# Kernel tuning notes

Hardware: AMD Instinct MI355X
Metric: run time of the kernel (lower is better)

Reference implementation:

```python
import jax, jax.numpy as jnp
import numpy as np
import math

S, D = 8192, 128

def setup_inputs() -> dict:
    key = jax.random.key(0)
    kq, kk, kv = jax.random.split(key, 3)
    return {
        "q": jax.random.normal(kq, (S, D), dtype=jnp.float32),
        "k": jax.random.normal(kk, (S, D), dtype=jnp.float32),
        "v": jax.random.normal(kv, (S, D), dtype=jnp.float32),
    }

def reference(q, k, v):
    # scores: [S, S]; scale by sqrt(d) as in the torch module
    scale = 1.0 / math.sqrt(q.shape[1])
    scores = (q @ k.T) * scale
    attn = jax.nn.softmax(scores, axis=-1)
    return attn @ v
```

## Files before the change

### kernel.cpp

```cpp
#include <hip/hip_runtime.h>
#include <hip/hip_bf16.h>

#define SEQ 8192
#define HD 128
#define BM 128
#define BN 64
#define NQT (SEQ / BM)
#define THREADS 512

typedef __bf16 bf16_t;
typedef __bf16 bf16x2 __attribute__((ext_vector_type(2)));
typedef __bf16 bf16x8 __attribute__((ext_vector_type(8)));
typedef float f32x4 __attribute__((ext_vector_type(4)));
typedef float f32x16 __attribute__((ext_vector_type(16)));
typedef unsigned int u32x4 __attribute__((ext_vector_type(4)));

#if __has_builtin(__builtin_amdgcn_exp2f)
__device__ inline float exp2_fast(float x) { return __builtin_amdgcn_exp2f(x); }
#else
__device__ inline float exp2_fast(float x) { return exp2f(x); }
#endif

__device__ inline void load_lds16(const void* g, void* l) {
  __builtin_amdgcn_global_load_lds(
      (const __attribute__((address_space(1))) void*)g,
      (__attribute__((address_space(3))) void*)l, 16, 0, 0);
}

__global__ __launch_bounds__(256) void prep_kernel(const float* __restrict__ K,
                                                   const float* __restrict__ V,
                                                   bf16_t* __restrict__ Kb,
                                                   bf16_t* __restrict__ VT) {
  const int b = (int)blockIdx.x;
  const int tid = (int)threadIdx.x;
  if (b < 256) {
    __shared__ float tile[64][65];
    const int T = b & 127;
    const int d0 = (b >> 7) * 64;
    const int s0 = T * 64;
    const int r = tid >> 2;
    const int c0 = (tid & 3) * 16;
#pragma unroll
    for (int j4 = 0; j4 < 4; ++j4) {
      float4 x = *(const float4*)&V[(size_t)(s0 + r) * HD + d0 + c0 + j4 * 4];
      tile[r][c0 + j4 * 4 + 0] = x.x;
      tile[r][c0 + j4 * 4 + 1] = x.y;
      tile[r][c0 + j4 * 4 + 2] = x.z;
      tile[r][c0 + j4 * 4 + 3] = x.w;
    }
    __syncthreads();
    const int d_l = tid & 63;
    const int kc0 = (tid >> 6) * 2;
#pragma unroll
    for (int k2 = 0; k2 < 2; ++k2) {
      const int kc = kc0 + k2;
      bf16x8 wv;
#pragma unroll
      for (int j = 0; j < 8; ++j) wv[j] = (bf16_t)tile[kc * 8 + j][d_l];
      *(bf16x8*)&VT[((size_t)(T * 8 + kc) * 128 + d0 + d_l) * 8] = wv;
    }
  } else {
    const int base = (b - 256) * 2048 + tid * 8;
    const int row = base >> 7;
    const int c = (base >> 3) & 15;
    const int T = row >> 6;
    const int r = row & 63;
    float4 a = *(const float4*)&K[base];
    float4 cc = *(const float4*)&K[base + 4];
    bf16x8 f;
    f[0] = (bf16_t)a.x; f[1] = (bf16_t)a.y; f[2] = (bf16_t)a.z; f[3] = (bf16_t)a.w;
    f[4] = (bf16_t)cc.x; f[5] = (bf16_t)cc.y; f[6] = (bf16_t)cc.z; f[7] = (bf16_t)cc.w;
    *(bf16x8*)&Kb[((size_t)(T * 16 + c) * 64 + r) * 8] = f;
  }
}

__global__ __launch_bounds__(THREADS, 4) void fattn_kernel(
    const float* __restrict__ Q, const bf16_t* __restrict__ Kb,
    const bf16_t* __restrict__ VT, float* __restrict__ Opart,
    float* __restrict__ Lpart, int kshift, int nit) {
  __shared__ __align__(16) bf16_t kt2[2][16][64][8];
  __shared__ __align__(16) bf16_t vt2[2][8][128][8];
  __shared__ __align__(16) char pbuf[4][4][64][16];

  const int tid = (int)threadIdx.x;
  const int lane = tid & 63;
  const int w = tid >> 6;
  const int qw = w & 3;
  const int g = w >> 2;
  const int h = lane >> 5;
  const int n32 = lane & 31;

  const int qt = (int)blockIdx.x >> kshift;
  const int sp = (int)blockIdx.x & ((1 << kshift) - 1);
  const int qbase = qt * BM;
  const int tile0 = sp * nit;

  const float SC2 = 0.08838834764831845f * 1.4426950408889634f;

  bf16x8 qf[8];
  {
    const float* qp = Q + (size_t)(qbase + qw * 32 + n32) * HD + h * 8;
#pragma unroll
    for (int kk = 0; kk < 8; ++kk) {
      float4 a = *(const float4*)(qp + kk * 16);
      float4 b = *(const float4*)(qp + kk * 16 + 4);
      bf16x8 f;
      f[0] = (bf16_t)(a.x * SC2); f[1] = (bf16_t)(a.y * SC2);
      f[2] = (bf16_t)(a.z * SC2); f[3] = (bf16_t)(a.w * SC2);
      f[4] = (bf16_t)(b.x * SC2); f[5] = (bf16_t)(b.y * SC2);
      f[6] = (bf16_t)(b.z * SC2); f[7] = (bf16_t)(b.w * SC2);
      qf[kk] = f;
    }
  }

  f32x16 o_acc[2];
#pragma unroll
  for (int i = 0; i < 2; ++i)
#pragma unroll
    for (int e = 0; e < 16; ++e) o_acc[i][e] = 0.f;
  float l_acc = 0.f;

  const int rr0 = w * 2;

#pragma unroll
  for (int t = 0; t < 2; ++t) {
    const int rr = rr0 + t;
    load_lds16(Kb + ((size_t)(tile0 * 16 + rr) * 64 + lane) * 8,
               (char*)&kt2[0][0][0][0] + rr * 1024);
    load_lds16(VT + ((size_t)(tile0 * 8 + (rr >> 1)) * 128 + (rr & 1) * 64 + lane) * 8,
               (char*)&vt2[0][0][0][0] + rr * 1024);
  }
  __syncthreads();

  for (int it = 0; it < nit; ++it) {
    const int cur = it & 1;
    const int nxt = cur ^ 1;
    const int ntile = tile0 + ((it + 1 < nit) ? it + 1 : 0);
#pragma unroll
    for (int t = 0; t < 2; ++t) {
      const int rr = rr0 + t;
      load_lds16(Kb + ((size_t)(ntile * 16 + rr) * 64 + lane) * 8,
                 (char*)&kt2[nxt][0][0][0] + rr * 1024);
      load_lds16(VT + ((size_t)(ntile * 8 + (rr >> 1)) * 128 + (rr & 1) * 64 + lane) * 8,
                 (char*)&vt2[nxt][0][0][0] + rr * 1024);
    }

    f32x16 sacc;
#pragma unroll
    for (int e = 0; e < 16; ++e) sacc[e] = 0.f;
#pragma unroll
    for (int kk = 0; kk < 8; ++kk) {
      bf16x8 af = *(const bf16x8*)&kt2[cur][2 * kk + h][g * 32 + n32][0];
      sacc = __builtin_amdgcn_mfma_f32_32x32x16_bf16(af, qf[kk], sacc, 0, 0, 0);
    }

#pragma unroll
    for (int kk2 = 0; kk2 < 2; ++kk2) {
      float pf[8];
#pragma unroll
      for (int j = 0; j < 8; ++j) pf[j] = exp2_fast(sacc[8 * kk2 + j]);
#pragma unroll
      for (int j = 0; j < 8; ++j) l_acc += pf[j];
      bf16x2 p0, p1, p2, p3;
      p0[0] = (bf16_t)pf[0]; p0[1] = (bf16_t)pf[1];
      p1[0] = (bf16_t)pf[2]; p1[1] = (bf16_t)pf[3];
      p2[0] = (bf16_t)pf[4]; p2[1] = (bf16_t)pf[5];
      p3[0] = (bf16_t)pf[6]; p3[1] = (bf16_t)pf[7];
      const unsigned int sA = __builtin_bit_cast(unsigned int, p0);
      const unsigned int sB = __builtin_bit_cast(unsigned int, p1);
      const unsigned int sC = __builtin_bit_cast(unsigned int, p2);
      const unsigned int sD = __builtin_bit_cast(unsigned int, p3);
      unsigned int s0 = h ? sA : sC, s1 = h ? sB : sD;
      unsigned int r0 = __shfl_xor(s0, 32);
      unsigned int r1 = __shfl_xor(s1, 32);
      unsigned int o0 = h ? sC : sA, o1 = h ? sD : sB;
      u32x4 fv;
      fv[0] = h ? r0 : o0; fv[1] = h ? r1 : o1;
      fv[2] = h ? o0 : r0; fv[3] = h ? o1 : r1;
      *(u32x4*)&pbuf[qw][g * 2 + kk2][lane][0] = fv;
    }
    __syncthreads();

#pragma unroll
    for (int C = 0; C < 4; ++C) {
      bf16x8 pa = *(const bf16x8*)&pbuf[qw][C][h * 32 + n32][0];
#pragma unroll
      for (int ot = 0; ot < 2; ++ot) {
        bf16x8 vb = *(const bf16x8*)&vt2[cur][C * 2 + h][g * 64 + ot * 32 + n32][0];
        o_acc[ot] = __builtin_amdgcn_mfma_f32_32x32x16_bf16(pa, vb, o_acc[ot], 0, 0, 0);
      }
    }

    __syncthreads();
  }

  {
    float* op = Opart + ((size_t)sp * SEQ + qbase + qw * 32) * HD + g * 64;
#pragma unroll
    for (int ot = 0; ot < 2; ++ot)
#pragma unroll
      for (int reg = 0; reg < 16; ++reg) {
        const int row = (reg & 3) + 8 * (reg >> 2) + 4 * h;
        op[row * HD + ot * 32 + n32] = o_acc[ot][reg];
      }
    float l = l_acc + __shfl_xor(l_acc, 32);
    float* lfb = (float*)pbuf;
    if (lane < 32) lfb[g * 128 + qw * 32 + n32] = l;
    __syncthreads();
    if (g == 0 && lane < 32)
      Lpart[(size_t)sp * SEQ + qbase + qw * 32 + n32] =
          l + lfb[128 + qw * 32 + n32];
  }
}

__global__ __launch_bounds__(256) void combine_kernel(const float* __restrict__ Opart,
                                                      const float* __restrict__ Lpart,
                                                      float* __restrict__ out, int ksplit) {
  const int tid = (int)threadIdx.x;
  const int row = (int)blockIdx.x * 8 + (tid >> 5);
  const int c0 = (tid & 31) * 4;
  float lsum = 0.f;
  for (int s = 0; s < ksplit; ++s) lsum += Lpart[(size_t)s * SEQ + row];
  f32x4 acc;
#pragma unroll
  for (int e = 0; e < 4; ++e) acc[e] = 0.f;
  for (int s = 0; s < ksplit; ++s) {
    f32x4 o = *(const f32x4*)&Opart[((size_t)s * SEQ + row) * HD + c0];
#pragma unroll
    for (int e = 0; e < 4; ++e) acc[e] += o[e];
  }
  const float inv = 1.0f / lsum;
  f32x4 res;
#pragma unroll
  for (int e = 0; e < 4; ++e) res[e] = acc[e] * inv;
  *(f32x4*)&out[(size_t)row * HD + c0] = res;
}

extern "C" void kernel_launch(void* const* d_in, const int* in_sizes, int n_in,
                              void* d_out, int out_size, void* d_ws, size_t ws_size,
                              hipStream_t stream) {
  const float* Q = (const float*)d_in[0];
  const float* K = (const float*)d_in[1];
  const float* V = (const float*)d_in[2];
  float* out = (float*)d_out;

  int ksplit = 8, kshift = 3;
  while (ksplit > 1) {
    size_t need = (size_t)ksplit * SEQ * HD * 4
                + (size_t)ksplit * SEQ * 4
                + (size_t)SEQ * HD * 2 * 2;
    if (need <= ws_size) break;
    ksplit >>= 1; kshift--;
  }

  char* ws = (char*)d_ws;
  float* Opart = (float*)ws;
  float* Lpart = (float*)(ws + (size_t)ksplit * SEQ * HD * 4);
  bf16_t* Kb = (bf16_t*)(ws + (size_t)ksplit * SEQ * HD * 4 + (size_t)ksplit * SEQ * 4);
  bf16_t* VT = Kb + (size_t)SEQ * HD;

  const int nit = SEQ / (ksplit * BN);

  prep_kernel<<<768, 256, 0, stream>>>(K, V, Kb, VT);
  fattn_kernel<<<NQT * ksplit, THREADS, 0, stream>>>(Q, Kb, VT, Opart, Lpart, kshift, nit);
  combine_kernel<<<SEQ / 8, 256, 0, stream>>>(Opart, Lpart, out, ksplit);
}
```

Baseline: 116.0 us.

## Double query tile per block so each wave reuses K/V fragments for two query subtiles

Grows the query tile per block from 128 to 256 rows. Each wave now holds two 32-row Q fragment sets and issues two MFMAs per loaded K and V fragment, which halves LDS and global traffic for K/V per unit of work. To keep enough blocks in flight, the key split goes from 8 to 16 and launch bounds drop to 2 blocks per CU. The loop also uses precomputed pointer increments, skips the redundant prefetch on the last iteration, and replaces the first barrier with an explicit lgkmcnt wait plus s_barrier. The trade-offs are higher register pressure and more partial-output traffic for the combine step.

```diff
diff --git a/kernel.cpp b/kernel.cpp
--- a/kernel.cpp
+++ b/kernel.cpp
@@ -3,7 +3,7 @@
 
 #define SEQ 8192
 #define HD 128
-#define BM 128
+#define BM 256
 #define BN 64
 #define NQT (SEQ / BM)
 #define THREADS 512
@@ -74,18 +74,18 @@
   }
 }
 
-__global__ __launch_bounds__(THREADS, 4) void fattn_kernel(
+__global__ __launch_bounds__(THREADS, 2) void fattn_kernel(
     const float* __restrict__ Q, const bf16_t* __restrict__ Kb,
     const bf16_t* __restrict__ VT, float* __restrict__ Opart,
     float* __restrict__ Lpart, int kshift, int nit) {
   __shared__ __align__(16) bf16_t kt2[2][16][64][8];
   __shared__ __align__(16) bf16_t vt2[2][8][128][8];
-  __shared__ __align__(16) char pbuf[4][4][64][16];
+  __shared__ __align__(16) char pbuf[8][4][64][16];
 
   const int tid = (int)threadIdx.x;
   const int lane = tid & 63;
   const int w = tid >> 6;
-  const int qw = w & 3;
+  const int qp = w & 3;
   const int g = w >> 2;
   const int h = lane >> 5;
   const int n32 = lane & 31;
@@ -97,119 +97,164 @@
 
   const float SC2 = 0.08838834764831845f * 1.4426950408889634f;
 
-  bf16x8 qf[8];
-  {
-    const float* qp = Q + (size_t)(qbase + qw * 32 + n32) * HD + h * 8;
+  bf16x8 qf[2][8];
+#pragma unroll
+  for (int t = 0; t < 2; ++t) {
+    const float* qp_ = Q + (size_t)(qbase + (qp * 2 + t) * 32 + n32) * HD + h * 8;
 #pragma unroll
     for (int kk = 0; kk < 8; ++kk) {
-      float4 a = *(const float4*)(qp + kk * 16);
-      float4 b = *(const float4*)(qp + kk * 16 + 4);
+      float4 a = *(const float4*)(qp_ + kk * 16);
+      float4 b = *(const float4*)(qp_ + kk * 16 + 4);
       bf16x8 f;
       f[0] = (bf16_t)(a.x * SC2); f[1] = (bf16_t)(a.y * SC2);
       f[2] = (bf16_t)(a.z * SC2); f[3] = (bf16_t)(a.w * SC2);
       f[4] = (bf16_t)(b.x * SC2); f[5] = (bf16_t)(b.y * SC2);
       f[6] = (bf16_t)(b.z * SC2); f[7] = (bf16_t)(b.w * SC2);
-      qf[kk] = f;
-    }
-  }
-
-  f32x16 o_acc[2];
-#pragma unroll
-  for (int i = 0; i < 2; ++i)
-#pragma unroll
-    for (int e = 0; e < 16; ++e) o_acc[i][e] = 0.f;
-  float l_acc = 0.f;
-
-  const int rr0 = w * 2;
-
-#pragma unroll
-  for (int t = 0; t < 2; ++t) {
-    const int rr = rr0 + t;
-    load_lds16(Kb + ((size_t)(tile0 * 16 + rr) * 64 + lane) * 8,
-               (char*)&kt2[0][0][0][0] + rr * 1024);
-    load_lds16(VT + ((size_t)(tile0 * 8 + (rr >> 1)) * 128 + (rr & 1) * 64 + lane) * 8,
-               (char*)&vt2[0][0][0][0] + rr * 1024);
+      qf[t][kk] = f;
+    }
+  }
+
+  f32x16 o_acc[2][2];
+#pragma unroll
+  for (int t = 0; t < 2; ++t)
+#pragma unroll
+    for (int ot = 0; ot < 2; ++ot)
+#pragma unroll
+      for (int e = 0; e < 16; ++e) o_acc[t][ot][e] = 0.f;
+  float l_acc[2] = {0.f, 0.f};
+
+  const bf16_t* ktb = &kt2[0][h][g * 32 + n32][0];
+  const bf16_t* vtb = &vt2[0][h][g * 64 + n32][0];
+  char* pw[2];
+  const char* pr[2];
+#pragma unroll
+  for (int t = 0; t < 2; ++t) {
+    pw[t] = &pbuf[qp * 2 + t][g * 2][lane][0];
+    pr[t] = &pbuf[qp * 2 + t][0][h * 32 + n32][0];
+  }
+
+  const bf16_t* ksrc[2];
+  const bf16_t* vsrc[2];
+  char* kdst[2];
+  char* vdst[2];
+#pragma unroll
+  for (int t = 0; t < 2; ++t) {
+    const int rr = w * 2 + t;
+    ksrc[t] = Kb + ((size_t)(tile0 * 16 + rr) * 64 + lane) * 8;
+    vsrc[t] = VT + ((size_t)(tile0 * 8 + (rr >> 1)) * 128 + (rr & 1) * 64 + lane) * 8;
+    kdst[t] = (char*)&kt2[0][0][0][0] + rr * 1024;
+    vdst[t] = (char*)&vt2[0][0][0][0] + rr * 1024;
+  }
+
+#pragma unroll
+  for (int t = 0; t < 2; ++t) {
+    load_lds16(ksrc[t], kdst[t]);
+    load_lds16(vsrc[t], vdst[t]);
+    ksrc[t] += 8192;
+    vsrc[t] += 8192;
   }
   __syncthreads();
 
+  int bo = 0;
+  int nb = 16384;
+
   for (int it = 0; it < nit; ++it) {
-    const int cur = it & 1;
-    const int nxt = cur ^ 1;
-    const int ntile = tile0 + ((it + 1 < nit) ? it + 1 : 0);
+    if (it + 1 < nit) {
+#pragma unroll
+      for (int t = 0; t < 2; ++t) {
+        load_lds16(ksrc[t], kdst[t] + nb);
+        load_lds16(vsrc[t], vdst[t] + nb);
+        ksrc[t] += 8192;
+        vsrc[t] += 8192;
+      }
+    }
+
+    const bf16_t* kc_ = ktb + bo;
+    f32x16 sacc[2];
+#pragma unroll
+    for (int t = 0; t < 2; ++t)
+#pragma unroll
+      for (int e = 0; e < 16; ++e) sacc[t][e] = 0.f;
+#pragma unroll
+    for (int kk = 0; kk < 8; ++kk) {
+      bf16x8 af = *(const bf16x8*)(kc_ + kk * 1024);
+      sacc[0] = __builtin_amdgcn_mfma_f32_32x32x16_bf16(af, qf[0][kk], sacc[0], 0, 0, 0);
+      sacc[1] = __builtin_amdgcn_mfma_f32_32x32x16_bf16(af, qf[1][kk], sacc[1], 0, 0, 0);
+    }
+
 #pragma unroll
     for (int t = 0; t < 2; ++t) {
-      const int rr = rr0 + t;
-      load_lds16(Kb + ((size_t)(ntile * 16 + rr) * 64 + lane) * 8,
-                 (char*)&kt2[nxt][0][0][0] + rr * 1024);
-      load_lds16(VT + ((size_t)(ntile * 8 + (rr >> 1)) * 128 + (rr & 1) * 64 + lane) * 8,
-                 (char*)&vt2[nxt][0][0][0] + rr * 1024);
-    }
-
-    f32x16 sacc;
-#pragma unroll
-    for (int e = 0; e < 16; ++e) sacc[e] = 0.f;
-#pragma unroll
-    for (int kk = 0; kk < 8; ++kk) {
-      bf16x8 af = *(const bf16x8*)&kt2[cur][2 * kk + h][g * 32 + n32][0];
-      sacc = __builtin_amdgcn_mfma_f32_32x32x16_bf16(af, qf[kk], sacc, 0, 0, 0);
-    }
-
-#pragma unroll
-    for (int kk2 = 0; kk2 < 2; ++kk2) {
-      float pf[8];
-#pragma unroll
-      for (int j = 0; j < 8; ++j) pf[j] = exp2_fast(sacc[8 * kk2 + j]);
-#pragma unroll
-      for (int j = 0; j < 8; ++j) l_acc += pf[j];
-      bf16x2 p0, p1, p2, p3;
-      p0[0] = (bf16_t)pf[0]; p0[1] = (bf16_t)pf[1];
-      p1[0] = (bf16_t)pf[2]; p1[1] = (bf16_t)pf[3];
-      p2[0] = (bf16_t)pf[4]; p2[1] = (bf16_t)pf[5];
-      p3[0] = (bf16_t)pf[6]; p3[1] = (bf16_t)pf[7];
-      const unsigned int sA = __builtin_bit_cast(unsigned int, p0);
-      const unsigned int sB = __builtin_bit_cast(unsigned int, p1);
-      const unsigned int sC = __builtin_bit_cast(unsigned int, p2);
-      const unsigned int sD = __builtin_bit_cast(unsigned int, p3);
-      unsigned int s0 = h ? sA : sC, s1 = h ? sB : sD;
-      unsigned int r0 = __shfl_xor(s0, 32);
-      unsigned int r1 = __shfl_xor(s1, 32);
-      unsigned int o0 = h ? sC : sA, o1 = h ? sD : sB;
-      u32x4 fv;
-      fv[0] = h ? r0 : o0; fv[1] = h ? r1 : o1;
-      fv[2] = h ? o0 : r0; fv[3] = h ? o1 : r1;
-      *(u32x4*)&pbuf[qw][g * 2 + kk2][lane][0] = fv;
-    }
+#pragma unroll
+      for (int kk2 = 0; kk2 < 2; ++kk2) {
+        float pf[8];
+#pragma unroll
+        for (int j = 0; j < 8; ++j) pf[j] = exp2_fast(sacc[t][8 * kk2 + j]);
+#pragma unroll
+        for (int j = 0; j < 8; ++j) l_acc[t] += pf[j];
+        bf16x2 p0, p1, p2, p3;
+        p0[0] = (bf16_t)pf[0]; p0[1] = (bf16_t)pf[1];
+        p1[0] = (bf16_t)pf[2]; p1[1] = (bf16_t)pf[3];
+        p2[0] = (bf16_t)pf[4]; p2[1] = (bf16_t)pf[5];
+        p3[0] = (bf16_t)pf[6]; p3[1] = (bf16_t)pf[7];
+        const unsigned int sA = __builtin_bit_cast(unsigned int, p0);
+        const unsigned int sB = __builtin_bit_cast(unsigned int, p1);
+        const unsigned int sC = __builtin_bit_cast(unsigned int, p2);
+        const unsigned int sD = __builtin_bit_cast(unsigned int, p3);
+        unsigned int s0 = h ? sA : sC, s1 = h ? sB : sD;
+        unsigned int r0 = __shfl_xor(s0, 32);
+        unsigned int r1 = __shfl_xor(s1, 32);
+        unsigned int o0 = h ? sC : sA, o1 = h ? sD : sB;
+        u32x4 fv;
+        fv[0] = h ? r0 : o0; fv[1] = h ? r1 : o1;
+        fv[2] = h ? o0 : r0; fv[3] = h ? o1 : r1;
+        *(u32x4*)(pw[t] + kk2 * 1024) = fv;
+      }
+    }
+
+    asm volatile("s_waitcnt lgkmcnt(0)\n\ts_barrier" ::: "memory");
+
+    const bf16_t* vc_ = vtb + bo;
+#pragma unroll
+    for (int C = 0; C < 4; ++C) {
+      bf16x8 pa0 = *(const bf16x8*)(pr[0] + C * 1024);
+      bf16x8 pa1 = *(const bf16x8*)(pr[1] + C * 1024);
+#pragma unroll
+      for (int ot = 0; ot < 2; ++ot) {
+        bf16x8 vb = *(const bf16x8*)(vc_ + C * 2048 + ot * 256);
+        o_acc[0][ot] = __builtin_amdgcn_mfma_f32_32x32x16_bf16(pa0, vb, o_acc[0][ot], 0, 0, 0);
+        o_acc[1][ot] = __builtin_amdgcn_mfma_f32_32x32x16_bf16(pa1, vb, o_acc[1][ot], 0, 0, 0);
+      }
+    }
+
     __syncthreads();
-
-#pragma unroll
-    for (int C = 0; C < 4; ++C) {
-      bf16x8 pa = *(const bf16x8*)&pbuf[qw][C][h * 32 + n32][0];
-#pragma unroll
-      for (int ot = 0; ot < 2; ++ot) {
-        bf16x8 vb = *(const bf16x8*)&vt2[cur][C * 2 + h][g * 64 + ot * 32 + n32][0];
-        o_acc[ot] = __builtin_amdgcn_mfma_f32_32x32x16_bf16(pa, vb, o_acc[ot], 0, 0, 0);
-      }
-    }
-
-    __syncthreads();
-  }
-
-  {
-    float* op = Opart + ((size_t)sp * SEQ + qbase + qw * 32) * HD + g * 64;
+    bo ^= 8192;
+    nb ^= 16384;
+  }
+
+#pragma unroll
+  for (int t = 0; t < 2; ++t) {
+    float* op = Opart + ((size_t)sp * SEQ + qbase + (qp * 2 + t) * 32) * HD + g * 64;
 #pragma unroll
     for (int ot = 0; ot < 2; ++ot)
 #pragma unroll
       for (int reg = 0; reg < 16; ++reg) {
         const int row = (reg & 3) + 8 * (reg >> 2) + 4 * h;
-        op[row * HD + ot * 32 + n32] = o_acc[ot][reg];
+        op[row * HD + ot * 32 + n32] = o_acc[t][ot][reg];
       }
-    float l = l_acc + __shfl_xor(l_acc, 32);
-    float* lfb = (float*)pbuf;
-    if (lane < 32) lfb[g * 128 + qw * 32 + n32] = l;
-    __syncthreads();
-    if (g == 0 && lane < 32)
-      Lpart[(size_t)sp * SEQ + qbase + qw * 32 + n32] =
-          l + lfb[128 + qw * 32 + n32];
+  }
+  float l0 = l_acc[0] + __shfl_xor(l_acc[0], 32);
+  float l1 = l_acc[1] + __shfl_xor(l_acc[1], 32);
+  float* lfb = (float*)pbuf;
+  if (lane < 32) {
+    lfb[g * 256 + (qp * 2 + 0) * 32 + n32] = l0;
+    lfb[g * 256 + (qp * 2 + 1) * 32 + n32] = l1;
+  }
+  __syncthreads();
+  if (g == 0 && lane < 32) {
+    Lpart[(size_t)sp * SEQ + qbase + (qp * 2 + 0) * 32 + n32] =
+        l0 + lfb[256 + (qp * 2 + 0) * 32 + n32];
+    Lpart[(size_t)sp * SEQ + qbase + (qp * 2 + 1) * 32 + n32] =
+        l1 + lfb[256 + (qp * 2 + 1) * 32 + n32];
   }
 }
 
@@ -244,7 +289,7 @@
   const float* V = (const float*)d_in[2];
   float* out = (float*)d_out;
 
-  int ksplit = 8, kshift = 3;
+  int ksplit = 16, kshift = 4;
   while (ksplit > 1) {
     size_t need = (size_t)ksplit * SEQ * HD * 4
                 + (size_t)ksplit * SEQ * 4
```

Measured after the change: 133.7 us. +15.3%, slower.

## Swap PV MFMA operands, reuse own P fragment, store transposed partial outputs

Applied to the files above, without the earlier changes.

The P·V product now uses V as the A operand and P as the B operand, so each wave reuses its own P fragment from registers and reads only the other half from LDS. The full __syncthreads before PV becomes an explicit waitcnt plus barrier. The main loop uses precomputed, pointer-incremented LDS and global addresses and skips the redundant prefetch on the last iteration. Partial outputs are written transposed (d-major), and the combine kernel transposes them back through a shared-memory tile. Together this trims address arithmetic and LDS traffic in the loop, at the cost of strided output stores and a heavier combine kernel.

```diff
diff --git a/kernel.cpp b/kernel.cpp
--- a/kernel.cpp
+++ b/kernel.cpp
@@ -76,7 +76,7 @@
 
 __global__ __launch_bounds__(THREADS, 4) void fattn_kernel(
     const float* __restrict__ Q, const bf16_t* __restrict__ Kb,
-    const bf16_t* __restrict__ VT, float* __restrict__ Opart,
+    const bf16_t* __restrict__ VT, float* __restrict__ OpartT,
     float* __restrict__ Lpart, int kshift, int nit) {
   __shared__ __align__(16) bf16_t kt2[2][16][64][8];
   __shared__ __align__(16) bf16_t vt2[2][8][128][8];
@@ -120,40 +120,55 @@
     for (int e = 0; e < 16; ++e) o_acc[i][e] = 0.f;
   float l_acc = 0.f;
 
-  const int rr0 = w * 2;
-
+  const bf16_t* ksrc[2];
+  const bf16_t* vsrc[2];
+  char* kdst[2];
+  char* vdst[2];
 #pragma unroll
   for (int t = 0; t < 2; ++t) {
-    const int rr = rr0 + t;
-    load_lds16(Kb + ((size_t)(tile0 * 16 + rr) * 64 + lane) * 8,
-               (char*)&kt2[0][0][0][0] + rr * 1024);
-    load_lds16(VT + ((size_t)(tile0 * 8 + (rr >> 1)) * 128 + (rr & 1) * 64 + lane) * 8,
-               (char*)&vt2[0][0][0][0] + rr * 1024);
+    const int rr = w * 2 + t;
+    ksrc[t] = Kb + ((size_t)(tile0 * 16 + rr) * 64 + lane) * 8;
+    vsrc[t] = VT + ((size_t)(tile0 * 8 + (rr >> 1)) * 128 + (rr & 1) * 64 + lane) * 8;
+    kdst[t] = (char*)&kt2[0][0][0][0] + rr * 1024;
+    vdst[t] = (char*)&vt2[0][0][0][0] + rr * 1024;
+  }
+
+#pragma unroll
+  for (int t = 0; t < 2; ++t) {
+    load_lds16(ksrc[t], kdst[t]);
+    load_lds16(vsrc[t], vdst[t]);
+    ksrc[t] += 8192;
+    vsrc[t] += 8192;
   }
   __syncthreads();
 
+  const bf16_t* ktb = &kt2[0][h][g * 32 + n32][0];
+  const bf16_t* vtbA = &vt2[0][h][g * 64 + n32][0];
+  int bo = 0;
+  int nb = 16384;
+
   for (int it = 0; it < nit; ++it) {
-    const int cur = it & 1;
-    const int nxt = cur ^ 1;
-    const int ntile = tile0 + ((it + 1 < nit) ? it + 1 : 0);
-#pragma unroll
-    for (int t = 0; t < 2; ++t) {
-      const int rr = rr0 + t;
-      load_lds16(Kb + ((size_t)(ntile * 16 + rr) * 64 + lane) * 8,
-                 (char*)&kt2[nxt][0][0][0] + rr * 1024);
-      load_lds16(VT + ((size_t)(ntile * 8 + (rr >> 1)) * 128 + (rr & 1) * 64 + lane) * 8,
-                 (char*)&vt2[nxt][0][0][0] + rr * 1024);
-    }
-
+    if (it + 1 < nit) {
+#pragma unroll
+      for (int t = 0; t < 2; ++t) {
+        load_lds16(ksrc[t], kdst[t] + nb);
+        load_lds16(vsrc[t], vdst[t] + nb);
+        ksrc[t] += 8192;
+        vsrc[t] += 8192;
+      }
+    }
+
+    const bf16_t* kc_ = ktb + bo;
     f32x16 sacc;
 #pragma unroll
     for (int e = 0; e < 16; ++e) sacc[e] = 0.f;
 #pragma unroll
     for (int kk = 0; kk < 8; ++kk) {
-      bf16x8 af = *(const bf16x8*)&kt2[cur][2 * kk + h][g * 32 + n32][0];
+      bf16x8 af = *(const bf16x8*)(kc_ + kk * 1024);
       sacc = __builtin_amdgcn_mfma_f32_32x32x16_bf16(af, qf[kk], sacc, 0, 0, 0);
     }
 
+    bf16x8 pown[2];
 #pragma unroll
     for (int kk2 = 0; kk2 < 2; ++kk2) {
       float pf[8];
@@ -177,63 +192,90 @@
       u32x4 fv;
       fv[0] = h ? r0 : o0; fv[1] = h ? r1 : o1;
       fv[2] = h ? o0 : r0; fv[3] = h ? o1 : r1;
+      pown[kk2] = __builtin_bit_cast(bf16x8, fv);
       *(u32x4*)&pbuf[qw][g * 2 + kk2][lane][0] = fv;
     }
-    __syncthreads();
-
-#pragma unroll
-    for (int C = 0; C < 4; ++C) {
-      bf16x8 pa = *(const bf16x8*)&pbuf[qw][C][h * 32 + n32][0];
-#pragma unroll
-      for (int ot = 0; ot < 2; ++ot) {
-        bf16x8 vb = *(const bf16x8*)&vt2[cur][C * 2 + h][g * 64 + ot * 32 + n32][0];
-        o_acc[ot] = __builtin_amdgcn_mfma_f32_32x32x16_bf16(pa, vb, o_acc[ot], 0, 0, 0);
+
+    asm volatile("s_waitcnt lgkmcnt(0)\n\ts_barrier" ::: "memory");
+
+    const bf16_t* vc_ = vtbA + bo;
+#pragma unroll
+    for (int c = 0; c < 4; ++c) {
+      bf16x8 pb = ((c >> 1) == g) ? pown[c & 1]
+                                  : *(const bf16x8*)&pbuf[qw][c][lane][0];
+#pragma unroll
+      for (int dt = 0; dt < 2; ++dt) {
+        bf16x8 av = *(const bf16x8*)(vc_ + (2 * c) * 1024 + dt * 256);
+        o_acc[dt] = __builtin_amdgcn_mfma_f32_32x32x16_bf16(av, pb, o_acc[dt], 0, 0, 0);
       }
     }
 
     __syncthreads();
+    bo ^= 8192;
+    nb ^= 16384;
   }
 
   {
-    float* op = Opart + ((size_t)sp * SEQ + qbase + qw * 32) * HD + g * 64;
-#pragma unroll
-    for (int ot = 0; ot < 2; ++ot)
+    float* op = OpartT + (size_t)sp * HD * SEQ + qbase + qw * 32 + n32;
+#pragma unroll
+    for (int dt = 0; dt < 2; ++dt)
 #pragma unroll
       for (int reg = 0; reg < 16; ++reg) {
-        const int row = (reg & 3) + 8 * (reg >> 2) + 4 * h;
-        op[row * HD + ot * 32 + n32] = o_acc[ot][reg];
+        const int d = g * 64 + dt * 32 + (reg & 3) + 8 * (reg >> 2) + 4 * h;
+        op[(size_t)d * SEQ] = o_acc[dt][reg];
       }
     float l = l_acc + __shfl_xor(l_acc, 32);
     float* lfb = (float*)pbuf;
     if (lane < 32) lfb[g * 128 + qw * 32 + n32] = l;
     __syncthreads();
     if (g == 0 && lane < 32)
-      Lpart[(size_t)sp * SEQ + qbase + qw * 32 + n32] =
-          l + lfb[128 + qw * 32 + n32];
-  }
-}
-
-__global__ __launch_bounds__(256) void combine_kernel(const float* __restrict__ Opart,
+      Lpart[(size_t)sp * SEQ + qbase + qw * 32 + n32] = l + lfb[128 + qw * 32 + n32];
+  }
+}
+
+__global__ __launch_bounds__(256) void combine_kernel(const float* __restrict__ OpartT,
                                                       const float* __restrict__ Lpart,
                                                       float* __restrict__ out, int ksplit) {
+  __shared__ float tile[64][68];
+  __shared__ float lbuf[64];
   const int tid = (int)threadIdx.x;
-  const int row = (int)blockIdx.x * 8 + (tid >> 5);
-  const int c0 = (tid & 31) * 4;
-  float lsum = 0.f;
-  for (int s = 0; s < ksplit; ++s) lsum += Lpart[(size_t)s * SEQ + row];
-  f32x4 acc;
-#pragma unroll
-  for (int e = 0; e < 4; ++e) acc[e] = 0.f;
-  for (int s = 0; s < ksplit; ++s) {
-    f32x4 o = *(const f32x4*)&Opart[((size_t)s * SEQ + row) * HD + c0];
-#pragma unroll
-    for (int e = 0; e < 4; ++e) acc[e] += o[e];
-  }
-  const float inv = 1.0f / lsum;
-  f32x4 res;
-#pragma unroll
-  for (int e = 0; e < 4; ++e) res[e] = acc[e] * inv;
-  *(f32x4*)&out[(size_t)row * HD + c0] = res;
+  const int q0 = (int)blockIdx.x * 64;
+  if (tid < 64) {
+    float s = 0.f;
+    for (int sp = 0; sp < ksplit; ++sp) s += Lpart[(size_t)sp * SEQ + q0 + tid];
+    lbuf[tid] = 1.0f / s;
+  }
+  __syncthreads();
+  const int dd = tid >> 2, qc = tid & 3;
+  const int q = tid >> 2, dc = tid & 3;
+  for (int db = 0; db < 2; ++db) {
+    f32x4 acc[4];
+#pragma unroll
+    for (int jj = 0; jj < 4; ++jj)
+#pragma unroll
+      for (int e = 0; e < 4; ++e) acc[jj][e] = 0.f;
+    for (int sp = 0; sp < ksplit; ++sp) {
+      const float* src = OpartT + ((size_t)sp * HD + db * 64 + dd) * SEQ + q0 + qc * 16;
+#pragma unroll
+      for (int jj = 0; jj < 4; ++jj) {
+        f32x4 v = *(const f32x4*)(src + jj * 4);
+#pragma unroll
+        for (int e = 0; e < 4; ++e) acc[jj][e] += v[e];
+      }
+    }
+#pragma unroll
+    for (int jj = 0; jj < 4; ++jj) *(f32x4*)&tile[dd][qc * 16 + jj * 4] = acc[jj];
+    __syncthreads();
+    const float inv = lbuf[q];
+#pragma unroll
+    for (int jj = 0; jj < 4; ++jj) {
+      f32x4 r;
+#pragma unroll
+      for (int i = 0; i < 4; ++i) r[i] = tile[dc * 16 + jj * 4 + i][q] * inv;
+      *(f32x4*)&out[(size_t)(q0 + q) * HD + db * 64 + dc * 16 + jj * 4] = r;
+    }
+    __syncthreads();
+  }
 }
 
 extern "C" void kernel_launch(void* const* d_in, const int* in_sizes, int n_in,
@@ -254,7 +296,7 @@
   }
 
   char* ws = (char*)d_ws;
-  float* Opart = (float*)ws;
+  float* OpartT = (float*)ws;
   float* Lpart = (float*)(ws + (size_t)ksplit * SEQ * HD * 4);
   bf16_t* Kb = (bf16_t*)(ws + (size_t)ksplit * SEQ * HD * 4 + (size_t)ksplit * SEQ * 4);
   bf16_t* VT = Kb + (size_t)SEQ * HD;
@@ -262,6 +304,6 @@
   const int nit = SEQ / (ksplit * BN);
 
   prep_kernel<<<768, 256, 0, stream>>>(K, V, Kb, VT);
-  fattn_kernel<<<NQT * ksplit, THREADS, 0, stream>>>(Q, Kb, VT, Opart, Lpart, kshift, nit);
-  combine_kernel<<<SEQ / 8, 256, 0, stream>>>(Opart, Lpart, out, ksplit);
-}
+  fattn_kernel<<<NQT * ksplit, THREADS, 0, stream>>>(Q, Kb, VT, OpartT, Lpart, kshift, nit);
+  combine_kernel<<<SEQ / 64, 256, 0, stream>>>(OpartT, Lpart, out, ksplit);
+}
```

New measurement: 123.1 us. +6.1%, slower.
